# Performance work log

Hardware: AMD Instinct MI355X
Metric: run time of the kernel (lower is better)

Reference implementation:

```python
import jax, jax.numpy as jnp
import numpy as np

D_MODEL = 1024
N_HEADS = 16
D_H = D_MODEL // N_HEADS
B, S = 2, 2048


def setup_inputs() -> dict:
    key = jax.random.key(0)
    ks = jax.random.split(key, 12)
    s = 1.0 / np.sqrt(D_MODEL)
    inp = {
        "Q": jax.random.normal(ks[0], (B, S, D_MODEL), jnp.float32),
        "K": jax.random.normal(ks[1], (B, S, D_MODEL), jnp.float32),
        "V": jax.random.normal(ks[2], (B, S, D_MODEL), jnp.float32),
        # causal mask: True means masked out (matches masked_fill semantics)
        "masked": jnp.broadcast_to(~jnp.tril(jnp.ones((S, S), bool)), (B, S, S)),
        "WQ_w": jax.random.uniform(ks[3], (D_MODEL, D_MODEL), jnp.float32, -s, s),
        "WQ_b": jax.random.uniform(ks[4], (D_MODEL,), jnp.float32, -s, s),
        "WK_w": jax.random.uniform(ks[5], (D_MODEL, D_MODEL), jnp.float32, -s, s),
        "WK_b": jax.random.uniform(ks[6], (D_MODEL,), jnp.float32, -s, s),
        "WV_w": jax.random.uniform(ks[7], (D_MODEL, D_MODEL), jnp.float32, -s, s),
        "WV_b": jax.random.uniform(ks[8], (D_MODEL,), jnp.float32, -s, s),
        "Wo_w": jax.random.uniform(ks[9], (D_MODEL, D_MODEL), jnp.float32, -s, s),
        "Wo_b": jax.random.uniform(ks[10], (D_MODEL,), jnp.float32, -s, s),
    }
    return inp


def reference(Q, K, V, masked, WQ_w, WQ_b, WK_w, WK_b, WV_w, WV_b, Wo_w, Wo_b):
    b = Q.shape[0]
    # torch Linear: y = x @ W^T + b
    def split_heads(x):
        return x.reshape(b, -1, N_HEADS, D_H).transpose(0, 2, 1, 3)  # [B,H,S,d_h]

    q = split_heads(Q @ WQ_w.T + WQ_b)
    k = split_heads(K @ WK_w.T + WK_b)
    v = split_heads(V @ WV_w.T + WV_b)

    scores = jnp.einsum("bhqd,bhkd->bhqk", q, k) / np.sqrt(D_H)
    scores = jnp.where(masked[:, None, :, :], jnp.float32(-1e9), scores)
    attn = jax.nn.softmax(scores, axis=-1)
    ctx = jnp.einsum("bhqk,bhkd->bhqd", attn, v)  # [B,H,S,d_h]
    ctx = ctx.transpose(0, 2, 1, 3).reshape(b, -1, N_HEADS * D_H)
    return ctx @ Wo_w.T + Wo_b
```

## Files before the change

kernel.cpp:

```cpp
#include <hip/hip_runtime.h>
#include <hip/hip_bf16.h>
#include <math.h>


typedef __bf16 bf16_t;
typedef bf16_t bf16x8 __attribute__((ext_vector_type(8)));
typedef bf16_t bf16x4 __attribute__((ext_vector_type(4)));
typedef float f32x4 __attribute__((ext_vector_type(4)));

#define MFMA16(a, b, c) __builtin_amdgcn_mfma_f32_16x16x32_bf16(a, b, c, 0, 0, 0)

constexpr int S_LEN = 2048;
constexpr int DMODEL = 1024;
constexpr int DHEAD = 64;
constexpr int MTOT = 2 * S_LEN;
constexpr size_t NQ = (size_t)MTOT * DMODEL;
constexpr size_t NW = (size_t)DMODEL * DMODEL;
constexpr float ESC = 0.18033688011112042f;

__device__ __forceinline__ void load_lds16(const void* g, void* l) {
  __builtin_amdgcn_global_load_lds((const __attribute__((address_space(1))) void*)g,
                                   (__attribute__((address_space(3))) void*)l, 16, 0, 0);
}

__device__ __forceinline__ void swap32(unsigned& a, unsigned& b) {
#if __has_builtin(__builtin_amdgcn_permlane32_swap)
  auto r = __builtin_amdgcn_permlane32_swap(a, b, false, false);
  a = r[0]; b = r[1];
#else
  asm volatile("s_nop 1\n\tv_permlane32_swap_b32 %0, %1\n\ts_nop 1"
               : "+v"(a), "+v"(b));
#endif
}
__device__ __forceinline__ void swap16(unsigned& a, unsigned& b) {
#if __has_builtin(__builtin_amdgcn_permlane16_swap)
  auto r = __builtin_amdgcn_permlane16_swap(a, b, false, false);
  a = r[0]; b = r[1];
#else
  asm volatile("s_nop 1\n\tv_permlane16_swap_b32 %0, %1\n\ts_nop 1"
               : "+v"(a), "+v"(b));
#endif
}

__device__ __forceinline__ float fexp2(float x) {
#if __has_builtin(__builtin_amdgcn_exp2f)
  return __builtin_amdgcn_exp2f(x);
#else
  float r;
  asm("v_exp_f32 %0, %1\n\ts_nop 1" : "=v"(r) : "v"(x));
  return r;
#endif
}

__global__ __launch_bounds__(256) void convert_w(
    const float* __restrict__ W0, const float* __restrict__ W1,
    const float* __restrict__ W2, const float* __restrict__ W3,
    bf16_t* __restrict__ dst) {
  const size_t i = ((size_t)blockIdx.x * 256 + threadIdx.x) * 4;
  const float* s;
  size_t off = i;
  if (off < NW) { s = W0; }
  else if (off < 2 * NW) { s = W1; off -= NW; }
  else if (off < 3 * NW) { s = W2; off -= 2 * NW; }
  else { s = W3; off -= 3 * NW; }
  const float4 v4 = *(const float4*)(s + off);
  bf16x4 b;
  b[0] = (bf16_t)v4.x; b[1] = (bf16_t)v4.y; b[2] = (bf16_t)v4.z; b[3] = (bf16_t)v4.w;
  *(bf16x4*)(dst + i) = b;
}

__global__ __launch_bounds__(256, 3) void gemm_qkv(const float* __restrict__ Qf,
                                                   const float* __restrict__ Kf,
                                                   const float* __restrict__ Vf,
                                                   const bf16_t* __restrict__ Wbase,
                                                   const float* __restrict__ b0,
                                                   const float* __restrict__ b1,
                                                   const float* __restrict__ b2,
                                                   bf16_t* __restrict__ obase) {
  __shared__ bf16_t As[128 * 64];
  __shared__ bf16_t Ws[128 * 64];
  const int z = blockIdx.z;
  const int bm = blockIdx.x * 128, bn = blockIdx.y * 128;
  const int lane = threadIdx.x & 63, wave = threadIdx.x >> 6;
  const int col = lane & 15, quad = lane >> 4;
  const int wm = (wave >> 1) * 64, wn = (wave & 1) * 64;
  const int srow8 = lane >> 3, g8 = (lane & 7) ^ srow8;

  f32x4 acc[4][4];
#pragma unroll
  for (int i = 0; i < 4; i++)
#pragma unroll
    for (int j = 0; j < 4; j++)
#pragma unroll
      for (int r = 0; r < 4; r++) acc[i][j][r] = 0.f;

  const float* Af = ((z == 0) ? Qf : (z == 1) ? Kf : Vf) + (size_t)bm * 1024;
  const bf16_t* Wb = Wbase + z * NW + (size_t)bn * 1024;
  const float* bias = (z == 0) ? b0 : ((z == 1) ? b1 : b2);
  bf16_t* out = obase + z * NQ;

  f32x4 pre[8];
  auto grloadA = [&](int k0) {
#pragma unroll
    for (int i = 0; i < 4; i++) {
      const int rbase = (i * 4 + wave) * 8;
      const float* src = Af + (size_t)(rbase + srow8) * 1024 + k0 + g8 * 8;
      pre[2 * i] = *(const f32x4*)src;
      pre[2 * i + 1] = *(const f32x4*)(src + 4);
    }
  };

  grloadA(0);
  for (int k0 = 0; k0 < 1024; k0 += 64) {
    __syncthreads();
#pragma unroll
    for (int i = 0; i < 4; i++) {
      const int rbase = (i * 4 + wave) * 8;
      bf16x8 pk;
#pragma unroll
      for (int j = 0; j < 4; j++) {
        pk[j] = (bf16_t)pre[2 * i][j];
        pk[4 + j] = (bf16_t)pre[2 * i + 1][j];
      }
      *(bf16x8*)&As[rbase * 64 + lane * 8] = pk;
      load_lds16(Wb + (size_t)(rbase + srow8) * 1024 + k0 + g8 * 8, Ws + rbase * 64);
    }
    __syncthreads();
    if (k0 + 64 < 1024) grloadA(k0 + 64);
#pragma unroll
    for (int kc = 0; kc < 2; kc++) {
      const int slot = (kc * 4 + quad) ^ (col & 7);
      bf16x8 af[4], wf[4];
#pragma unroll
      for (int i = 0; i < 4; i++) af[i] = *(const bf16x8*)&As[(wm + i * 16 + col) * 64 + slot * 8];
#pragma unroll
      for (int j = 0; j < 4; j++) wf[j] = *(const bf16x8*)&Ws[(wn + j * 16 + col) * 64 + slot * 8];
#pragma unroll
      for (int i = 0; i < 4; i++)
#pragma unroll
        for (int j = 0; j < 4; j++) acc[i][j] = MFMA16(af[i], wf[j], acc[i][j]);
    }
  }

  const float esc = (z == 0) ? ESC : 1.0f;
#pragma unroll
  for (int i = 0; i < 4; i++) {
#pragma unroll
    for (int j = 0; j < 4; j++) {
      const int n = bn + wn + j * 16 + col;
      const float bv = bias[n];
      const int h = n >> 6, dh = n & 63;
      if (z < 2) {
#pragma unroll
        for (int r = 0; r < 4; r++) {
          const int m = bm + wm + i * 16 + quad * 4 + r;
          const int b = m >> 11, s = m & 2047;
          out[((size_t)((b * 16 + h) * S_LEN + s) << 6) | dh] =
              (bf16_t)((acc[i][j][r] + bv) * esc);
        }
      } else {
        const int m0 = bm + wm + i * 16 + quad * 4;
        const int b = m0 >> 11, s0 = m0 & 2047;
        bf16x4 p4;
#pragma unroll
        for (int r = 0; r < 4; r++) p4[r] = (bf16_t)(acc[i][j][r] + bv);
        *(bf16x4*)&out[(((size_t)((b * 16 + h) * DHEAD + dh)) << 11) | s0] = p4;
      }
    }
  }
}

__global__ __launch_bounds__(256, 2) void gemm_out(const bf16_t* __restrict__ A,
                                                   const bf16_t* __restrict__ W,
                                                   const float* __restrict__ bias,
                                                   float* __restrict__ out) {
  __shared__ bf16_t As[64 * 64];
  __shared__ bf16_t Ws[128 * 64];
  const int bm = blockIdx.x * 64, bn = blockIdx.y * 128;
  const int lane = threadIdx.x & 63, wave = threadIdx.x >> 6;
  const int col = lane & 15, quad = lane >> 4;
  const int wm = (wave >> 1) * 32, wn = (wave & 1) * 64;

  f32x4 acc[2][4];
#pragma unroll
  for (int i = 0; i < 2; i++)
#pragma unroll
    for (int j = 0; j < 4; j++)
#pragma unroll
      for (int r = 0; r < 4; r++) acc[i][j][r] = 0.f;

  const int srow = lane >> 3, s7 = lane & 7;
  const bf16_t* Ab = A + (size_t)bm * 1024;
  const bf16_t* Wb = W + (size_t)bn * 1024;

  for (int k0 = 0; k0 < 1024; k0 += 64) {
    __syncthreads();
#pragma unroll
    for (int i = 0; i < 2; i++) {
      const int rbase = (i * 4 + wave) * 8;
      const int g = s7 ^ srow;
      load_lds16(Ab + (size_t)(rbase + srow) * 1024 + k0 + g * 8, As + rbase * 64);
    }
#pragma unroll
    for (int i = 0; i < 4; i++) {
      const int rbase = (i * 4 + wave) * 8;
      const int g = s7 ^ srow;
      load_lds16(Wb + (size_t)(rbase + srow) * 1024 + k0 + g * 8, Ws + rbase * 64);
    }
    __syncthreads();
#pragma unroll
    for (int kc = 0; kc < 2; kc++) {
      const int slot = (kc * 4 + quad) ^ (col & 7);
      bf16x8 af[2], wf[4];
#pragma unroll
      for (int i = 0; i < 2; i++) af[i] = *(const bf16x8*)&As[(wm + i * 16 + col) * 64 + slot * 8];
#pragma unroll
      for (int j = 0; j < 4; j++) wf[j] = *(const bf16x8*)&Ws[(wn + j * 16 + col) * 64 + slot * 8];
#pragma unroll
      for (int i = 0; i < 2; i++)
#pragma unroll
        for (int j = 0; j < 4; j++) acc[i][j] = MFMA16(af[i], wf[j], acc[i][j]);
    }
  }

#pragma unroll
  for (int i = 0; i < 2; i++)
#pragma unroll
    for (int j = 0; j < 4; j++) {
      const int n = bn + wn + j * 16 + col;
      const float bv = bias[n];
#pragma unroll
      for (int r = 0; r < 4; r++) {
        const int m = bm + wm + i * 16 + quad * 4 + r;
        out[(size_t)m * DMODEL + n] = acc[i][j][r] + bv;
      }
    }
}

__global__ __launch_bounds__(256, 2) void attn(const bf16_t* __restrict__ q,
                                               const bf16_t* __restrict__ k,
                                               const bf16_t* __restrict__ vT,
                                               bf16_t* __restrict__ ctx,
                                               float* __restrict__ pO,
                                               float* __restrict__ pL) {
  const int bh = blockIdx.x;
  const int p = blockIdx.y;
  const int s = blockIdx.z;
  const int tB = 15 - p;
  const int nA = s ? 0 : (2 * p + 2);
  const int cB0 = s ? (15 - 2 * p) : 0;
  const int lane = threadIdx.x & 63, wave = threadIdx.x >> 6;
  const int col = lane & 15, quad = lane >> 4;
  const int qrel = wave * 16 + col;

  __shared__ bf16_t Ks[2][64 * 64];
  __shared__ bf16_t Vs[2][64 * 64];

  const bf16_t* kbh = k + (size_t)bh * S_LEN * DHEAD;
  const bf16_t* vbh = vT + (size_t)bh * DHEAD * S_LEN;

  const int srow8 = lane >> 3, s7 = lane & 7;
  const int g8 = s7 ^ srow8;

  auto stage = [&](int c, int b) {
#pragma unroll
    for (int i = 0; i < 2; i++) {
      const int rbase = (i * 4 + wave) * 8;
      load_lds16(kbh + (size_t)(c * 64 + rbase + srow8) * DHEAD + g8 * 8,
                 &Ks[b][rbase * 64]);
    }
#pragma unroll
    for (int i = 0; i < 2; i++) {
      const int dbase = (i * 4 + wave) * 8;
      load_lds16(vbh + (size_t)(dbase + srow8) * S_LEN + c * 64 + g8 * 8,
                 &Vs[b][dbase * 64]);
    }
  };

  bf16x8 aqw[2][2];
  f32x4 o0[4], o1[4], lacc0, lacc1;
  const f32x4 Zv = {0.f, 0.f, 0.f, 0.f};

  auto setup = [&](int tile_) {
    const int tq = tile_ ? tB : p;
    const bf16_t* qb = q + ((size_t)bh * S_LEN + tq * 128 + qrel) * DHEAD;
    aqw[0][0] = *(const bf16x8*)(qb + quad * 8);
    aqw[0][1] = *(const bf16x8*)(qb + 32 + quad * 8);
    aqw[1][0] = *(const bf16x8*)(qb + (size_t)64 * DHEAD + quad * 8);
    aqw[1][1] = *(const bf16x8*)(qb + (size_t)64 * DHEAD + 32 + quad * 8);
#pragma unroll
    for (int r = 0; r < 4; r++) { lacc0[r] = 0.f; lacc1[r] = 0.f; }
#pragma unroll
    for (int db = 0; db < 4; db++)
#pragma unroll
      for (int r = 0; r < 4; r++) { o0[db][r] = 0.f; o1[db][r] = 0.f; }
  };

  auto expw = [&](const f32x4& sv, int nb, bool dmask, f32x4& lac,
                  unsigned& w0, unsigned& w1) {
    union { bf16x4 v; unsigned u[2]; } pw;
#pragma unroll
    for (int r = 0; r < 4; r++) {
      float pv = fexp2(sv[r]);
      if (dmask && (nb * 16 + quad * 4 + r) > qrel) pv = 0.f;
      lac[r] += pv;
      pw.v[r] = (bf16_t)pv;
    }
    w0 = pw.u[0]; w1 = pw.u[1];
  };

  int tile = (0 >= nA) ? 1 : 0;
  stage(cB0, 0);
  int buf = 0;

#pragma unroll 1
  for (int i = 0; i < 17; ++i) {
    const bool inB = (i >= nA);
    const int c = inB ? (cB0 + i - nA) : i;
    const int cm = inB ? (2 * tB + 1) : (2 * p + 1);

    if (i == 0) setup(inB ? 1 : 0);
    else if (i == nA) setup(1);

    __syncthreads();

    if (i < 16) {
      const int i1 = i + 1;
      const int c1 = (i1 < nA) ? i1 : (cB0 + i1 - nA);
      stage(c1, buf ^ 1);
    }

    const bool skip0 = (c == cm);
    const bool mask0 = (c == cm - 1);
    const bool mask1 = (c == cm);

    f32x4 s0[4], s1[4];
    {
      const int sl = quad ^ (col & 7);
      bf16x8 kf[4];
#pragma unroll
      for (int nb = 0; nb < 4; nb++)
        kf[nb] = *(const bf16x8*)&Ks[buf][(nb * 16 + col) * 64 + sl * 8];
      __builtin_amdgcn_s_setprio(1);
      if (!skip0) {
#pragma unroll
        for (int nb = 0; nb < 4; nb++) s0[nb] = MFMA16(kf[nb], aqw[0][0], Zv);
      }
#pragma unroll
      for (int nb = 0; nb < 4; nb++) s1[nb] = MFMA16(kf[nb], aqw[1][0], Zv);
      __builtin_amdgcn_s_setprio(0);
    }
    {
      const int sl = (4 + quad) ^ (col & 7);
      bf16x8 kf[4];
#pragma unroll
      for (int nb = 0; nb < 4; nb++)
        kf[nb] = *(const bf16x8*)&Ks[buf][(nb * 16 + col) * 64 + sl * 8];
      __builtin_amdgcn_s_setprio(1);
      if (!skip0) {
#pragma unroll
        for (int nb = 0; nb < 4; nb++) s0[nb] = MFMA16(kf[nb], aqw[0][1], s0[nb]);
      }
#pragma unroll
      for (int nb = 0; nb < 4; nb++) s1[nb] = MFMA16(kf[nb], aqw[1][1], s1[nb]);
      __builtin_amdgcn_s_setprio(0);
    }

#pragma unroll
    for (int kcp = 0; kcp < 2; kcp++) {
      const int sl = (kcp * 4 + quad) ^ (col & 7);
      bf16x8 bv[4];
#pragma unroll
      for (int db = 0; db < 4; db++)
        bv[db] = *(const bf16x8*)&Vs[buf][(db * 16 + col) * 64 + sl * 8];

      union { unsigned u[4]; bf16x8 v; } pa1, pa0;
      {
        unsigned X0, X1, Y0, Y1;
        expw(s1[2 * kcp], 2 * kcp, mask1, lacc1, X0, X1);
        expw(s1[2 * kcp + 1], 2 * kcp + 1, mask1, lacc1, Y0, Y1);
        swap32(X0, Y0); swap16(X0, Y0);
        swap32(X1, Y1); swap16(X1, Y1);
        pa1.u[0] = X0; pa1.u[1] = X1; pa1.u[2] = Y0; pa1.u[3] = Y1;
      }
      if (!skip0) {
        unsigned X0, X1, Y0, Y1;
        expw(s0[2 * kcp], 2 * kcp, mask0, lacc0, X0, X1);
        expw(s0[2 * kcp + 1], 2 * kcp + 1, mask0, lacc0, Y0, Y1);
        swap32(X0, Y0); swap16(X0, Y0);
        swap32(X1, Y1); swap16(X1, Y1);
        pa0.u[0] = X0; pa0.u[1] = X1; pa0.u[2] = Y0; pa0.u[3] = Y1;
      }
      __builtin_amdgcn_s_setprio(1);
      if (!skip0) {
#pragma unroll
        for (int db = 0; db < 4; db++) o0[db] = MFMA16(bv[db], pa0.v, o0[db]);
      }
#pragma unroll
      for (int db = 0; db < 4; db++) o1[db] = MFMA16(bv[db], pa1.v, o1[db]);
      __builtin_amdgcn_s_setprio(0);
    }

    if (i == nA - 1) {
      float l0 = lacc0[0] + lacc0[1] + lacc0[2] + lacc0[3];
      l0 += __shfl_xor(l0, 16); l0 += __shfl_xor(l0, 32);
      float l1 = lacc1[0] + lacc1[1] + lacc1[2] + lacc1[3];
      l1 += __shfl_xor(l1, 16); l1 += __shfl_xor(l1, 32);
      const float inv0 = 1.f / l0, inv1 = 1.f / l1;
      const int b = bh >> 4, h = bh & 15;
      bf16_t* cb0 = ctx + ((size_t)(b * S_LEN + p * 128 + qrel)) * DMODEL + h * DHEAD;
      bf16_t* cb1 = cb0 + (size_t)64 * DMODEL;
#pragma unroll
      for (int db = 0; db < 4; db++) {
        bf16x4 w0, w1;
#pragma unroll
        for (int r = 0; r < 4; r++) {
          w0[r] = (bf16_t)(o0[db][r] * inv0);
          w1[r] = (bf16_t)(o1[db][r] * inv1);
        }
        *(bf16x4*)&cb0[db * 16 + quad * 4] = w0;
        *(bf16x4*)&cb1[db * 16 + quad * 4] = w1;
      }
    }
    buf ^= 1;
  }

  float l0 = lacc0[0] + lacc0[1] + lacc0[2] + lacc0[3];
  l0 += __shfl_xor(l0, 16); l0 += __shfl_xor(l0, 32);
  float l1 = lacc1[0] + lacc1[1] + lacc1[2] + lacc1[3];
  l1 += __shfl_xor(l1, 16); l1 += __shfl_xor(l1, 32);
  const int slot = ((bh * 8 + p) << 1) | s;
  float* myO = pO + (size_t)slot * (128 * 64);
  float* myL = pL + slot * 128;
#pragma unroll
  for (int db = 0; db < 4; db++) {
    *(f32x4*)&myO[(size_t)qrel * 64 + db * 16 + quad * 4] = o0[db];
    *(f32x4*)&myO[(size_t)(64 + qrel) * 64 + db * 16 + quad * 4] = o1[db];
  }
  if (quad == 0) { myL[qrel] = l0; myL[64 + qrel] = l1; }
}

__global__ __launch_bounds__(256) void combine(const float* __restrict__ pO,
                                               const float* __restrict__ pL,
                                               bf16_t* __restrict__ ctx) {
  const int pair = blockIdx.x;
  const int bh = pair >> 3, p = pair & 7;
  const int tB = 15 - p;
  const int b = bh >> 4, h = bh & 15;
  const float* O0 = pO + (size_t)(pair * 2 + 0) * (128 * 64);
  const float* O1 = pO + (size_t)(pair * 2 + 1) * (128 * 64);
  const float* L0 = pL + (pair * 2 + 0) * 128;
  const float* L1 = pL + (pair * 2 + 1) * 128;
#pragma unroll
  for (int n = 0; n < 8; n++) {
    const int idx = n * 1024 + threadIdx.x * 4;
    const int r = idx >> 6, cdh = idx & 63;
    const f32x4 a = *(const f32x4*)&O0[idx];
    const f32x4 c4 = *(const f32x4*)&O1[idx];
    const float inv = 1.f / (L0[r] + L1[r]);
    bf16x4 w;
#pragma unroll
    for (int j = 0; j < 4; j++) w[j] = (bf16_t)((a[j] + c4[j]) * inv);
    *(bf16x4*)&ctx[((size_t)(b * S_LEN + tB * 128 + r)) * DMODEL + h * DHEAD + cdh] = w;
  }
}

extern "C" void kernel_launch(void* const* d_in, const int* in_sizes, int n_in,
                              void* d_out, int out_size, void* d_ws, size_t ws_size,
                              hipStream_t stream) {
  const float* Q = (const float*)d_in[0];
  const float* K = (const float*)d_in[1];
  const float* V = (const float*)d_in[2];
  const float* WQw = (const float*)d_in[4];
  const float* WQb = (const float*)d_in[5];
  const float* WKw = (const float*)d_in[6];
  const float* WKb = (const float*)d_in[7];
  const float* WVw = (const float*)d_in[8];
  const float* WVb = (const float*)d_in[9];
  const float* Wow = (const float*)d_in[10];
  const float* Wob = (const float*)d_in[11];

  bf16_t* base = (bf16_t*)d_ws;
  bf16_t* Wc = base + 3 * NQ;
  bf16_t* qp = base + 3 * NQ + 4 * NW;
  bf16_t* ctx = base;
  float* pO = (float*)(base + NQ);
  float* pL = (float*)(base + (NQ / 2));
  pL = (float*)(Wc + NW / 2);

  convert_w<<<dim3((unsigned)(4 * NW / 4 / 256)), dim3(256), 0, stream>>>(
      WQw, WKw, WVw, Wow, Wc);

  gemm_qkv<<<dim3(32, 8, 3), dim3(256), 0, stream>>>(Q, K, V, Wc, WQb, WKb, WVb, qp);
  attn<<<dim3(32, 8, 2), dim3(256), 0, stream>>>(qp, qp + NQ, qp + 2 * NQ, ctx, pO, pL);
  combine<<<dim3(256), dim3(256), 0, stream>>>(pO, pL, ctx);
  gemm_out<<<dim3(64, 8), dim3(256), 0, stream>>>(ctx, Wc + 3 * NW, Wob, (float*)d_out);
}
```

Measured before the change: 224.6 us.

## Double-buffer LDS tiles in QKV GEMM and raise MFMA wave priority

The QKV projection GEMM now keeps two LDS buffers for the A and W tiles. The next K-slice's global loads (A into registers, W via direct-to-LDS) are issued before the current slice's MFMAs, which cuts one barrier per iteration and overlaps memory with compute. The MFMA block is wrapped in s_setprio to favour math waves. The price is double the LDS and occupancy lowered from 3 to 2 blocks per SM, which could reduce latency hiding. A few unused variables are also tidied up.

```diff
diff --git a/kernel.cpp b/kernel.cpp
--- a/kernel.cpp
+++ b/kernel.cpp
@@ -69,7 +69,7 @@
   *(bf16x4*)(dst + i) = b;
 }
 
-__global__ __launch_bounds__(256, 3) void gemm_qkv(const float* __restrict__ Qf,
+__global__ __launch_bounds__(256, 2) void gemm_qkv(const float* __restrict__ Qf,
                                                    const float* __restrict__ Kf,
                                                    const float* __restrict__ Vf,
                                                    const bf16_t* __restrict__ Wbase,
@@ -77,8 +77,8 @@
                                                    const float* __restrict__ b1,
                                                    const float* __restrict__ b2,
                                                    bf16_t* __restrict__ obase) {
-  __shared__ bf16_t As[128 * 64];
-  __shared__ bf16_t Ws[128 * 64];
+  __shared__ bf16_t As[2][128 * 64];
+  __shared__ bf16_t Ws[2][128 * 64];
   const int z = blockIdx.z;
   const int bm = blockIdx.x * 128, bn = blockIdx.y * 128;
   const int lane = threadIdx.x & 63, wave = threadIdx.x >> 6;
@@ -109,10 +109,15 @@
       pre[2 * i + 1] = *(const f32x4*)(src + 4);
     }
   };
-
-  grloadA(0);
-  for (int k0 = 0; k0 < 1024; k0 += 64) {
-    __syncthreads();
+  auto stageW = [&](int k0, int b) {
+#pragma unroll
+    for (int i = 0; i < 4; i++) {
+      const int rbase = (i * 4 + wave) * 8;
+      load_lds16(Wb + (size_t)(rbase + srow8) * 1024 + k0 + g8 * 8,
+                 &Ws[b][rbase * 64]);
+    }
+  };
+  auto writeA = [&](int b) {
 #pragma unroll
     for (int i = 0; i < 4; i++) {
       const int rbase = (i * 4 + wave) * 8;
@@ -122,24 +127,42 @@
         pk[j] = (bf16_t)pre[2 * i][j];
         pk[4 + j] = (bf16_t)pre[2 * i + 1][j];
       }
-      *(bf16x8*)&As[rbase * 64 + lane * 8] = pk;
-      load_lds16(Wb + (size_t)(rbase + srow8) * 1024 + k0 + g8 * 8, Ws + rbase * 64);
-    }
-    __syncthreads();
-    if (k0 + 64 < 1024) grloadA(k0 + 64);
+      *(bf16x8*)&As[b][rbase * 64 + lane * 8] = pk;
+    }
+  };
+
+  grloadA(0);
+  stageW(0, 0);
+  writeA(0);
+  __syncthreads();
+  int buf = 0;
+
+  for (int k0 = 0; k0 < 1024; k0 += 64) {
+    const bool more = (k0 + 64 < 1024);
+    if (more) {
+      grloadA(k0 + 64);
+      stageW(k0 + 64, buf ^ 1);
+    }
 #pragma unroll
     for (int kc = 0; kc < 2; kc++) {
       const int slot = (kc * 4 + quad) ^ (col & 7);
       bf16x8 af[4], wf[4];
 #pragma unroll
-      for (int i = 0; i < 4; i++) af[i] = *(const bf16x8*)&As[(wm + i * 16 + col) * 64 + slot * 8];
-#pragma unroll
-      for (int j = 0; j < 4; j++) wf[j] = *(const bf16x8*)&Ws[(wn + j * 16 + col) * 64 + slot * 8];
-#pragma unroll
       for (int i = 0; i < 4; i++)
+        af[i] = *(const bf16x8*)&As[buf][(wm + i * 16 + col) * 64 + slot * 8];
+#pragma unroll
+      for (int j = 0; j < 4; j++)
+        wf[j] = *(const bf16x8*)&Ws[buf][(wn + j * 16 + col) * 64 + slot * 8];
+      __builtin_amdgcn_s_setprio(1);
+#pragma unroll
+      for (int i = 0; i < 4; i++)
 #pragma unroll
         for (int j = 0; j < 4; j++) acc[i][j] = MFMA16(af[i], wf[j], acc[i][j]);
-    }
+      __builtin_amdgcn_s_setprio(0);
+    }
+    if (more) writeA(buf ^ 1);
+    __syncthreads();
+    buf ^= 1;
   }
 
   const float esc = (z == 0) ? ESC : 1.0f;
@@ -309,7 +332,6 @@
     w0 = pw.u[0]; w1 = pw.u[1];
   };
 
-  int tile = (0 >= nA) ? 1 : 0;
   stage(cB0, 0);
   int buf = 0;
 
@@ -485,8 +507,7 @@
   bf16_t* qp = base + 3 * NQ + 4 * NW;
   bf16_t* ctx = base;
   float* pO = (float*)(base + NQ);
-  float* pL = (float*)(base + (NQ / 2));
-  pL = (float*)(Wc + NW / 2);
+  float* pL = (float*)(Wc + NW / 2);
 
   convert_w<<<dim3((unsigned)(4 * NW / 4 / 256)), dim3(256), 0, stream>>>(
       WQw, WKw, WVw, Wow, Wc);
```

Measured after the change: 242.7 us. +8.1%, slower.

## Fuse split-KV combine into output projection GEMM A-tile loading

Applied to the files above, without the earlier changes.

Removes the separate combine kernel. For row tiles whose context comes from split partial outputs, gemm_out now loads both fp32 partial O tiles and their row sums, normalises them, converts to bf16 and writes the result into LDS in place of the ctx tile. The next k-step's partials are prefetched into registers during the MFMA loop. This saves one launch and the ctx write/read round trip. In exchange, 8 GEMM column blocks each redo the same combine work, and those blocks carry more register pressure and fp32 traffic.

```diff
diff --git a/kernel.cpp b/kernel.cpp
--- a/kernel.cpp
+++ b/kernel.cpp
@@ -171,6 +171,8 @@
 }
 
 __global__ __launch_bounds__(256, 2) void gemm_out(const bf16_t* __restrict__ A,
+                                                   const float* __restrict__ pO,
+                                                   const float* __restrict__ pL,
                                                    const bf16_t* __restrict__ W,
                                                    const float* __restrict__ bias,
                                                    float* __restrict__ out) {
@@ -180,6 +182,17 @@
   const int lane = threadIdx.x & 63, wave = threadIdx.x >> 6;
   const int col = lane & 15, quad = lane >> 4;
   const int wm = (wave >> 1) * 32, wn = (wave & 1) * 64;
+  const int srow = lane >> 3, s7 = lane & 7;
+  const int g = s7 ^ srow;
+
+  const int tq = (bm >> 7) & 15;
+  const bool isB = (tq >= 8);
+  const int p = isB ? (15 - tq) : tq;
+  const int b = bm >> 11;
+  const int lr0 = (0 * 4 + wave) * 8 + srow;
+  const int lr1 = (1 * 4 + wave) * 8 + srow;
+  const int rt0 = (bm & 64) + lr0;
+  const int rt1 = (bm & 64) + lr1;
 
   f32x4 acc[2][4];
 #pragma unroll
@@ -189,25 +202,62 @@
 #pragma unroll
       for (int r = 0; r < 4; r++) acc[i][j][r] = 0.f;
 
-  const int srow = lane >> 3, s7 = lane & 7;
   const bf16_t* Ab = A + (size_t)bm * 1024;
   const bf16_t* Wb = W + (size_t)bn * 1024;
 
+  f32x4 preO[8];
+  float preL[4];
+  auto grloadO = [&](int k0) {
+    const int h = k0 >> 6;
+    const int pair = (b * 16 + h) * 8 + p;
+    const float* O0 = pO + (size_t)(pair * 2 + 0) * (128 * 64);
+    const float* O1 = pO + (size_t)(pair * 2 + 1) * (128 * 64);
+    const float* L0 = pL + (pair * 2 + 0) * 128;
+    const float* L1 = pL + (pair * 2 + 1) * 128;
+    preO[0] = *(const f32x4*)&O0[rt0 * 64 + g * 8];
+    preO[1] = *(const f32x4*)&O0[rt0 * 64 + g * 8 + 4];
+    preO[2] = *(const f32x4*)&O1[rt0 * 64 + g * 8];
+    preO[3] = *(const f32x4*)&O1[rt0 * 64 + g * 8 + 4];
+    preO[4] = *(const f32x4*)&O0[rt1 * 64 + g * 8];
+    preO[5] = *(const f32x4*)&O0[rt1 * 64 + g * 8 + 4];
+    preO[6] = *(const f32x4*)&O1[rt1 * 64 + g * 8];
+    preO[7] = *(const f32x4*)&O1[rt1 * 64 + g * 8 + 4];
+    preL[0] = L0[rt0]; preL[1] = L1[rt0];
+    preL[2] = L0[rt1]; preL[3] = L1[rt1];
+  };
+  auto writeAB = [&]() {
+#pragma unroll
+    for (int i = 0; i < 2; i++) {
+      const float inv = 1.f / (preL[2 * i] + preL[2 * i + 1]);
+      bf16x8 pk;
+#pragma unroll
+      for (int j = 0; j < 4; j++) {
+        pk[j] = (bf16_t)((preO[4 * i][j] + preO[4 * i + 2][j]) * inv);
+        pk[4 + j] = (bf16_t)((preO[4 * i + 1][j] + preO[4 * i + 3][j]) * inv);
+      }
+      *(bf16x8*)&As[(i * 4 + wave) * 8 * 64 + lane * 8] = pk;
+    }
+  };
+
+  if (isB) grloadO(0);
   for (int k0 = 0; k0 < 1024; k0 += 64) {
     __syncthreads();
-#pragma unroll
-    for (int i = 0; i < 2; i++) {
-      const int rbase = (i * 4 + wave) * 8;
-      const int g = s7 ^ srow;
-      load_lds16(Ab + (size_t)(rbase + srow) * 1024 + k0 + g * 8, As + rbase * 64);
+    if (isB) {
+      writeAB();
+    } else {
+#pragma unroll
+      for (int i = 0; i < 2; i++) {
+        const int rbase = (i * 4 + wave) * 8;
+        load_lds16(Ab + (size_t)(rbase + srow) * 1024 + k0 + g * 8, As + rbase * 64);
+      }
     }
 #pragma unroll
     for (int i = 0; i < 4; i++) {
       const int rbase = (i * 4 + wave) * 8;
-      const int g = s7 ^ srow;
       load_lds16(Wb + (size_t)(rbase + srow) * 1024 + k0 + g * 8, Ws + rbase * 64);
     }
     __syncthreads();
+    if (isB && k0 + 64 < 1024) grloadO(k0 + 64);
 #pragma unroll
     for (int kc = 0; kc < 2; kc++) {
       const int slot = (kc * 4 + quad) ^ (col & 7);
@@ -309,7 +359,6 @@
     w0 = pw.u[0]; w1 = pw.u[1];
   };
 
-  int tile = (0 >= nA) ? 1 : 0;
   stage(cB0, 0);
   int buf = 0;
 
@@ -438,31 +487,6 @@
     *(f32x4*)&myO[(size_t)(64 + qrel) * 64 + db * 16 + quad * 4] = o1[db];
   }
   if (quad == 0) { myL[qrel] = l0; myL[64 + qrel] = l1; }
-}
-
-__global__ __launch_bounds__(256) void combine(const float* __restrict__ pO,
-                                               const float* __restrict__ pL,
-                                               bf16_t* __restrict__ ctx) {
-  const int pair = blockIdx.x;
-  const int bh = pair >> 3, p = pair & 7;
-  const int tB = 15 - p;
-  const int b = bh >> 4, h = bh & 15;
-  const float* O0 = pO + (size_t)(pair * 2 + 0) * (128 * 64);
-  const float* O1 = pO + (size_t)(pair * 2 + 1) * (128 * 64);
-  const float* L0 = pL + (pair * 2 + 0) * 128;
-  const float* L1 = pL + (pair * 2 + 1) * 128;
-#pragma unroll
-  for (int n = 0; n < 8; n++) {
-    const int idx = n * 1024 + threadIdx.x * 4;
-    const int r = idx >> 6, cdh = idx & 63;
-    const f32x4 a = *(const f32x4*)&O0[idx];
-    const f32x4 c4 = *(const f32x4*)&O1[idx];
-    const float inv = 1.f / (L0[r] + L1[r]);
-    bf16x4 w;
-#pragma unroll
-    for (int j = 0; j < 4; j++) w[j] = (bf16_t)((a[j] + c4[j]) * inv);
-    *(bf16x4*)&ctx[((size_t)(b * S_LEN + tB * 128 + r)) * DMODEL + h * DHEAD + cdh] = w;
-  }
 }
 
 extern "C" void kernel_launch(void* const* d_in, const int* in_sizes, int n_in,
@@ -485,14 +509,13 @@
   bf16_t* qp = base + 3 * NQ + 4 * NW;
   bf16_t* ctx = base;
   float* pO = (float*)(base + NQ);
-  float* pL = (float*)(base + (NQ / 2));
-  pL = (float*)(Wc + NW / 2);
+  float* pL = (float*)(Wc + NW / 2);
 
   convert_w<<<dim3((unsigned)(4 * NW / 4 / 256)), dim3(256), 0, stream>>>(
       WQw, WKw, WVw, Wow, Wc);
 
   gemm_qkv<<<dim3(32, 8, 3), dim3(256), 0, stream>>>(Q, K, V, Wc, WQb, WKb, WVb, qp);
   attn<<<dim3(32, 8, 2), dim3(256), 0, stream>>>(qp, qp + NQ, qp + 2 * NQ, ctx, pO, pL);
-  combine<<<dim3(256), dim3(256), 0, stream>>>(pO, pL, ctx);
-  gemm_out<<<dim3(64, 8), dim3(256), 0, stream>>>(ctx, Wc + 3 * NW, Wob, (float*)d_out);
-}
+  gemm_out<<<dim3(64, 8), dim3(256), 0, stream>>>(ctx, pO, pL, Wc + 3 * NW, Wob,
+                                                  (float*)d_out);
+}
```

Result: no change. 225.7 us (+0.5%).
